# Kernel optimization log

Hardware: AMD Instinct MI355X
Metric: run time of the kernel (lower is better)

## Reference

```python
import jax, jax.numpy as jnp
import numpy as np

NUM_HEADS = 12

def setup_inputs() -> dict:
    key = jax.random.key(0)
    k1, k2, k3, k4 = jax.random.split(key, 4)
    B, N, D = 8, 1024, 768
    x = jax.random.normal(k1, (B, N, D), dtype=jnp.float32)
    mask = jax.random.randint(k2, (B, N), 0, 2, dtype=jnp.int32)
    Wqkv = jax.random.normal(k3, (3 * D, D), dtype=jnp.float32) * (D ** -0.5)
    Wproj = jax.random.normal(k4, (D, D), dtype=jnp.float32) * (D ** -0.5)
    bproj = jnp.zeros((D,), dtype=jnp.float32)
    return {"x": x, "mask": mask, "Wqkv": Wqkv, "Wproj": Wproj, "bproj": bproj}

def reference(x, mask, Wqkv, Wproj, bproj):
    B, N, D = x.shape
    H = NUM_HEADS
    hd = D // H
    scale = hd ** -0.5
    # QKV projection (no bias), split into q,k,v of shape [B,H,N,hd]
    qkv = jnp.einsum('bnd,ed->bne', x, Wqkv).reshape(B, N, 3, H, hd)
    qkv = jnp.transpose(qkv, (2, 0, 3, 1, 4))
    q, k, v = qkv[0], qkv[1], qkv[2]
    # padding mask: attend where both query and key are valid; masked-out
    # (padded) query rows attend only to themselves (diagonal) to avoid NaNs
    m = mask.astype(bool)  # [B,N]
    pair = m[:, None, :, None] & m[:, None, None, :]          # [B,1,N,N]
    diag = jnp.eye(N, dtype=bool)[None, None]                 # [1,1,N,N]
    attn_mask = pair | (diag & ~m[:, None, :, None])          # [B,1,N,N]
    scores = jnp.einsum('bhnd,bhmd->bhnm', q, k) * scale      # [B,H,N,N]
    scores = jnp.where(attn_mask, scores, jnp.finfo(scores.dtype).min)
    attn = jax.nn.softmax(scores, axis=-1)
    out = jnp.einsum('bhnm,bhmd->bhnd', attn, v)
    out = jnp.transpose(out, (0, 2, 1, 3)).reshape(B, N, D)
    out = jnp.einsum('bnd,ed->bne', out, Wproj) + bproj
    return out
```

## Files before the change

### kernel.cpp

```cpp
#include <hip/hip_runtime.h>
#include <hip/hip_bf16.h>
#include <stdint.h>


typedef unsigned short u16;
typedef __attribute__((ext_vector_type(8))) short short8;
typedef __attribute__((ext_vector_type(4))) float f32x4;

#define MFMA16(a, b, c) __builtin_amdgcn_mfma_f32_16x16x32_bf16((a), (b), (c), 0, 0, 0)

static __device__ __forceinline__ u16 f2bf(float f) {
    __hip_bfloat16 h = __float2bfloat16(f);
    return *(u16*)&h;
}
static __device__ __forceinline__ void gld16(const u16* g, u16* l) {
  __builtin_amdgcn_global_load_lds(
      (const __attribute__((address_space(1))) void*)g,
      (__attribute__((address_space(3))) void*)l, 16, 0, 0);
}

__global__ __launch_bounds__(256) void cvt_bf16(
    const float* __restrict__ s0, u16* __restrict__ d0, int n0,
    const float* __restrict__ s1, u16* __restrict__ d1, int n1,
    const float* __restrict__ s2, u16* __restrict__ d2, int n2) {
  int i = (blockIdx.x * 256 + threadIdx.x) * 4;
  const float* s; u16* d;
  if (i < n0) { s = s0 + i; d = d0 + i; }
  else if ((i -= n0) < n1) { s = s1 + i; d = d1 + i; }
  else if ((i -= n1) < n2) { s = s2 + i; d = d2 + i; }
  else return;
  float4 v = *(const float4*)s;
  ushort4 o;
  o.x = f2bf(v.x); o.y = f2bf(v.y); o.z = f2bf(v.z); o.w = f2bf(v.w);
  *(ushort4*)d = o;
}

template<int K, int BN, int LDC, bool BF16OUT>
__global__ __launch_bounds__(256) void gemm_bt(
    const u16* __restrict__ A,
    const u16* __restrict__ B,
    void* __restrict__ Cout,
    const float* __restrict__ bias) {
  constexpr int NT = BN / 32;
  __shared__ u16 As[128 * 64];
  __shared__ u16 Bs[BN * 64];
  const int tid = threadIdx.x;
  const int w = tid >> 6, l = tid & 63;
  const int lane16 = l & 15, quad = l >> 4;
  const int i0 = blockIdx.y * 128, j0 = blockIdx.x * BN;
  const int mh = (w & 1) * 64;
  const int nh = (w >> 1) * (BN / 2);

  f32x4 acc[4][NT];
  #pragma unroll
  for (int mt = 0; mt < 4; mt++)
    #pragma unroll
    for (int nt = 0; nt < NT; nt++) acc[mt][nt] = (f32x4){0.f, 0.f, 0.f, 0.f};

  for (int kt = 0; kt < K / 64; kt++) {
    const int k0 = kt * 64;
    __syncthreads();
    #pragma unroll
    for (int s = 0; s < 4; s++) {
      int idx = tid + s * 256;
      int row = idx >> 3, c8 = (idx & 7) * 8;
      gld16(&A[(size_t)(i0 + row) * K + k0 + c8], &As[idx * 8]);
    }
    #pragma unroll
    for (int s = 0; s < BN / 32; s++) {
      int idx = tid + s * 256;
      int row = idx >> 3, c8 = (idx & 7) * 8;
      gld16(&B[(size_t)(j0 + row) * K + k0 + c8], &Bs[idx * 8]);
    }
    __syncthreads();

    #pragma unroll
    for (int ks = 0; ks < 2; ks++) {
      short8 af[4], bf[NT];
      #pragma unroll
      for (int mt = 0; mt < 4; mt++)
        af[mt] = *(const short8*)&As[(mh + mt * 16 + lane16) * 64 + ks * 32 + quad * 8];
      #pragma unroll
      for (int nt = 0; nt < NT; nt++)
        bf[nt] = *(const short8*)&Bs[(nh + nt * 16 + lane16) * 64 + ks * 32 + quad * 8];
      #pragma unroll
      for (int mt = 0; mt < 4; mt++)
        #pragma unroll
        for (int nt = 0; nt < NT; nt++)
          acc[mt][nt] = MFMA16(af[mt], bf[nt], acc[mt][nt]);
    }
  }

  #pragma unroll
  for (int mt = 0; mt < 4; mt++) {
    #pragma unroll
    for (int nt = 0; nt < NT; nt++) {
      int col = j0 + nh + nt * 16 + lane16;
      #pragma unroll
      for (int r = 0; r < 4; r++) {
        int row = i0 + mh + mt * 16 + quad * 4 + r;
        if (BF16OUT) {
          ((u16*)Cout)[(size_t)row * LDC + col] = f2bf(acc[mt][nt][r]);
        } else {
          ((float*)Cout)[(size_t)row * LDC + col] = acc[mt][nt][r] + bias[col];
        }
      }
    }
  }
}

__global__ __launch_bounds__(256, 3) void attn_mfma(
    const u16* __restrict__ qkv,
    const int* __restrict__ mask,
    u16* __restrict__ ctx) {
  __shared__ u16 Ks[64][72];
  __shared__ u16 Vt[64][72];
  __shared__ u16 Ps[4][32][72];
  __shared__ float mkb_all[1024];

  const int tid = threadIdx.x;
  const int w = tid >> 6, l = tid & 63;
  const int lane16 = l & 15, quad = l >> 4;
  const int idx = blockIdx.x;
  const int bh = idx % 96;
  const int rb = idx / 96;
  const int b = bh / 12, h = bh % 12;
  const int n0 = rb * 128;
  const int baseRow = b * 1024;

  const int key_s = tid >> 2, ds_s = (tid & 3) * 16;
  const int kA_s = (tid & 31) * 2, dg_s = tid >> 5;

  {
    int4 mv = *(const int4*)&mask[baseRow + tid * 4];
    f32x4 mf;
    mf[0] = mv.x ? 0.f : -1e38f;
    mf[1] = mv.y ? 0.f : -1e38f;
    mf[2] = mv.z ? 0.f : -1e38f;
    mf[3] = mv.w ? 0.f : -1e38f;
    *(f32x4*)&mkb_all[tid * 4] = mf;
  }

  short8 qfrag[2][2];
  #pragma unroll
  for (int qt = 0; qt < 2; qt++) {
    const u16* qp = qkv + (size_t)(baseRow + n0 + w*32 + qt*16 + lane16) * 2304 + h*64;
    #pragma unroll
    for (int ks = 0; ks < 2; ks++)
      qfrag[qt][ks] = *(const short8*)(qp + ks*32 + quad*8);
  }

  f32x4 oacc[2][4];
  #pragma unroll
  for (int qt = 0; qt < 2; qt++)
    #pragma unroll
    for (int nt = 0; nt < 4; nt++) oacc[qt][nt] = (f32x4){0.f, 0.f, 0.f, 0.f};
  f32x4 lsum4[2] = {(f32x4){0.f,0.f,0.f,0.f}, (f32x4){0.f,0.f,0.f,0.f}};

  const float K1 = 0.18033688011112043f;
  const float K0 = -23.083120654223415f;

  uint4 kr0, kr1, vr0, vr1;
  {
    const u16* kp = qkv + (size_t)(baseRow + key_s) * 2304 + 768 + h*64 + ds_s;
    kr0 = *(const uint4*)kp;
    kr1 = *(const uint4*)(kp + 8);
    const u16* vp = qkv + (size_t)(baseRow + kA_s) * 2304 + 1536 + h*64 + dg_s*8;
    vr0 = *(const uint4*)vp;
    vr1 = *(const uint4*)(vp + 2304);
  }

  for (int c = 0; c < 16; c++) {
    if (c) __syncthreads();

    *(uint4*)&Ks[key_s][ds_s]     = kr0;
    *(uint4*)&Ks[key_s][ds_s + 8] = kr1;
    {
      const u16* va = (const u16*)&vr0;
      const u16* vb = (const u16*)&vr1;
      #pragma unroll
      for (int j = 0; j < 8; j++)
        *(unsigned int*)&Vt[dg_s*8 + j][kA_s] =
            (unsigned int)va[j] | ((unsigned int)vb[j] << 16);
    }

    if (c + 1 < 16) {
      const u16* kp = qkv + (size_t)(baseRow + (c+1)*64 + key_s) * 2304 + 768 + h*64 + ds_s;
      kr0 = *(const uint4*)kp;
      kr1 = *(const uint4*)(kp + 8);
      const u16* vp = qkv + (size_t)(baseRow + (c+1)*64 + kA_s) * 2304 + 1536 + h*64 + dg_s*8;
      vr0 = *(const uint4*)vp;
      vr1 = *(const uint4*)(vp + 2304);
    }
    __syncthreads();

    f32x4 sacc[4][2];
    #pragma unroll
    for (int kt = 0; kt < 4; kt++)
      #pragma unroll
      for (int qt = 0; qt < 2; qt++) sacc[kt][qt] = (f32x4){0.f, 0.f, 0.f, 0.f};
    #pragma unroll
    for (int ks = 0; ks < 2; ks++) {
      short8 kf[4];
      #pragma unroll
      for (int kt = 0; kt < 4; kt++)
        kf[kt] = *(const short8*)&Ks[kt*16 + lane16][ks*32 + quad*8];
      __builtin_amdgcn_s_setprio(1);
      #pragma unroll
      for (int kt = 0; kt < 4; kt++)
        #pragma unroll
        for (int qt = 0; qt < 2; qt++)
          sacc[kt][qt] = MFMA16(kf[kt], qfrag[qt][ks], sacc[kt][qt]);
      __builtin_amdgcn_s_setprio(0);
    }

    #pragma unroll
    for (int kt = 0; kt < 4; kt++) {
      f32x4 mk4 = *(const f32x4*)&mkb_all[c*64 + kt*16 + quad*4];
      #pragma unroll
      for (int qt = 0; qt < 2; qt++) {
        u16 pk[4];
        #pragma unroll
        for (int r = 0; r < 4; r++) {
          float e = __builtin_amdgcn_exp2f(fmaf(sacc[kt][qt][r], K1, K0) + mk4[r]);
          lsum4[qt][r] += e;
          pk[r] = f2bf(e);
        }
        uint2 pv;
        pv.x = (unsigned int)pk[0] | ((unsigned int)pk[1] << 16);
        pv.y = (unsigned int)pk[2] | ((unsigned int)pk[3] << 16);
        *(uint2*)&Ps[w][qt*16 + lane16][kt*16 + quad*4] = pv;
      }
    }

    #pragma unroll
    for (int kc = 0; kc < 2; kc++) {
      short8 pf[2], vf[4];
      #pragma unroll
      for (int qt = 0; qt < 2; qt++)
        pf[qt] = *(const short8*)&Ps[w][qt*16 + lane16][kc*32 + quad*8];
      #pragma unroll
      for (int nt = 0; nt < 4; nt++)
        vf[nt] = *(const short8*)&Vt[nt*16 + lane16][kc*32 + quad*8];
      __builtin_amdgcn_s_setprio(1);
      #pragma unroll
      for (int qt = 0; qt < 2; qt++)
        #pragma unroll
        for (int nt = 0; nt < 4; nt++)
          oacc[qt][nt] = MFMA16(pf[qt], vf[nt], oacc[qt][nt]);
      __builtin_amdgcn_s_setprio(0);
    }
  }

  float linv[2][4];
  #pragma unroll
  for (int qt = 0; qt < 2; qt++) {
    float s = lsum4[qt][0] + lsum4[qt][1] + lsum4[qt][2] + lsum4[qt][3];
    s += __shfl_xor(s, 16);
    s += __shfl_xor(s, 32);
    #pragma unroll
    for (int r = 0; r < 4; r++)
      linv[qt][r] = 1.0f / __shfl(s, quad*4 + r);
  }
  #pragma unroll
  for (int qt = 0; qt < 2; qt++) {
    #pragma unroll
    for (int r = 0; r < 4; r++) {
      int rl = w*32 + qt*16 + quad*4 + r;
      int rg = n0 + rl;
      int mq = (mkb_all[n0 + rl] == 0.f);
      #pragma unroll
      for (int nt = 0; nt < 4; nt++) {
        u16 outv;
        if (mq) {
          outv = f2bf(oacc[qt][nt][r] * linv[qt][r]);
        } else {
          outv = qkv[(size_t)(baseRow + rg) * 2304 + 1536 + h*64 + nt*16 + lane16];
        }
        ctx[(size_t)(baseRow + rg) * 768 + h*64 + nt*16 + lane16] = outv;
      }
    }
  }
}

extern "C" void kernel_launch(void* const* d_in, const int* in_sizes, int n_in,
                              void* d_out, int out_size, void* d_ws, size_t ws_size,
                              hipStream_t stream) {
  const float* x     = (const float*)d_in[0];
  const int*   mask  = (const int*)d_in[1];
  const float* Wqkv  = (const float*)d_in[2];
  const float* Wproj = (const float*)d_in[3];
  const float* bproj = (const float*)d_in[4];
  float* out = (float*)d_out;

  const int NX = 8192 * 768;
  const int NQ = 2304 * 768;
  const int NP = 768 * 768;

  char* wsb = (char*)d_ws;
  u16* qkv    = (u16*)wsb;
  u16* ctx    = (u16*)(wsb + (size_t)8192 * 2304 * 2);
  u16* xb     = (u16*)(wsb + (size_t)8192 * 2304 * 2 + (size_t)8192 * 768 * 2);
  u16* wqkvb  = xb + NX;
  u16* wprojb = wqkvb + NQ;

  int cvt_blocks = ((NX + NQ + NP) / 4 + 255) / 256;
  cvt_bf16<<<dim3(cvt_blocks), 256, 0, stream>>>(x, xb, NX, Wqkv, wqkvb, NQ, Wproj, wprojb, NP);

  gemm_bt<768, 128, 2304, true><<<dim3(18, 64), 256, 0, stream>>>(xb, wqkvb, qkv, nullptr);
  attn_mfma<<<dim3(768), 256, 0, stream>>>(qkv, mask, ctx);
  gemm_bt<768, 64, 768, false><<<dim3(12, 64), 256, 0, stream>>>(ctx, wprojb, out, bproj);
}
```

Measured before the change: 206.5 us.

## Double-buffer GEMM shared-memory tiles to overlap global loads with MFMA

Splits each 64-wide K tile of the GEMM into two 32-wide halves held in separate LDS buffers. The load of the next half is issued before computing on the current half, so global-to-LDS transfers overlap with MFMA work. This hides load latency that was previously exposed between barriers. In exchange, each K step is smaller and adds barriers, and the row stride drops to 32 elements, which may change LDS bank conflicts.

```diff
diff --git a/kernel.cpp b/kernel.cpp
--- a/kernel.cpp
+++ b/kernel.cpp
@@ -42,8 +42,10 @@
     void* __restrict__ Cout,
     const float* __restrict__ bias) {
   constexpr int NT = BN / 32;
-  __shared__ u16 As[128 * 64];
-  __shared__ u16 Bs[BN * 64];
+  __shared__ u16 As0[128 * 32];
+  __shared__ u16 Bs0[BN * 32];
+  __shared__ u16 As1[128 * 32];
+  __shared__ u16 Bs1[BN * 32];
   const int tid = threadIdx.x;
   const int w = tid >> 6, l = tid & 63;
   const int lane16 = l & 15, quad = l >> 4;
@@ -57,38 +59,45 @@
     #pragma unroll
     for (int nt = 0; nt < NT; nt++) acc[mt][nt] = (f32x4){0.f, 0.f, 0.f, 0.f};
 
-  for (int kt = 0; kt < K / 64; kt++) {
-    const int k0 = kt * 64;
+  auto stage = [&](u16* Ad, u16* Bd, int k0) {
+    #pragma unroll
+    for (int s = 0; s < 2; s++) {
+      int idx = tid + s * 256;
+      int row = idx >> 2, c8 = (idx & 3) * 8;
+      gld16(&A[(size_t)(i0 + row) * K + k0 + c8], &Ad[idx * 8]);
+    }
+    #pragma unroll
+    for (int s = 0; s < BN / 64; s++) {
+      int idx = tid + s * 256;
+      int row = idx >> 2, c8 = (idx & 3) * 8;
+      gld16(&B[(size_t)(j0 + row) * K + k0 + c8], &Bd[idx * 8]);
+    }
+  };
+  auto compute = [&](const u16* Asb, const u16* Bsb) {
+    short8 af[4], bf[NT];
+    #pragma unroll
+    for (int mt = 0; mt < 4; mt++)
+      af[mt] = *(const short8*)&Asb[(mh + mt * 16 + lane16) * 32 + quad * 8];
+    #pragma unroll
+    for (int nt = 0; nt < NT; nt++)
+      bf[nt] = *(const short8*)&Bsb[(nh + nt * 16 + lane16) * 32 + quad * 8];
+    #pragma unroll
+    for (int mt = 0; mt < 4; mt++)
+      #pragma unroll
+      for (int nt = 0; nt < NT; nt++)
+        acc[mt][nt] = MFMA16(af[mt], bf[nt], acc[mt][nt]);
+  };
+
+  stage(As0, Bs0, 0);
+  __syncthreads();
+  for (int kt2 = 0; kt2 < K / 64; kt2++) {
+    const int k0 = kt2 * 64;
+    stage(As1, Bs1, k0 + 32);
+    compute(As0, Bs0);
     __syncthreads();
-    #pragma unroll
-    for (int s = 0; s < 4; s++) {
-      int idx = tid + s * 256;
-      int row = idx >> 3, c8 = (idx & 7) * 8;
-      gld16(&A[(size_t)(i0 + row) * K + k0 + c8], &As[idx * 8]);
-    }
-    #pragma unroll
-    for (int s = 0; s < BN / 32; s++) {
-      int idx = tid + s * 256;
-      int row = idx >> 3, c8 = (idx & 7) * 8;
-      gld16(&B[(size_t)(j0 + row) * K + k0 + c8], &Bs[idx * 8]);
-    }
+    if (k0 + 64 < K) stage(As0, Bs0, k0 + 64);
+    compute(As1, Bs1);
     __syncthreads();
-
-    #pragma unroll
-    for (int ks = 0; ks < 2; ks++) {
-      short8 af[4], bf[NT];
-      #pragma unroll
-      for (int mt = 0; mt < 4; mt++)
-        af[mt] = *(const short8*)&As[(mh + mt * 16 + lane16) * 64 + ks * 32 + quad * 8];
-      #pragma unroll
-      for (int nt = 0; nt < NT; nt++)
-        bf[nt] = *(const short8*)&Bs[(nh + nt * 16 + lane16) * 64 + ks * 32 + quad * 8];
-      #pragma unroll
-      for (int mt = 0; mt < 4; mt++)
-        #pragma unroll
-        for (int nt = 0; nt < NT; nt++)
-          acc[mt][nt] = MFMA16(af[mt], bf[nt], acc[mt][nt]);
-    }
   }
 
   #pragma unroll
```

After: 202.4 us. About the same (-2.0%).
